# Kernel tuning notes

Hardware: AMD Instinct MI355X
Metric: run time of the kernel (lower is better)

Reference implementation:

```python
import jax, jax.numpy as jnp
import numpy as np

N_NODES = 50000
N_EDGES = 1600000
IN_DIM, HID_DIM, OUT_DIM, HEADS = 128, 128, 64, 8
NEG_SLOPE = 0.2
BN_EPS = 1e-5


def setup_inputs() -> dict:
    key = jax.random.key(0)
    ks = jax.random.split(key, 12)
    hpc = HID_DIM // HEADS  # per-head channels of layer 1
    return {
        "x": jax.random.normal(ks[0], (N_NODES, IN_DIM), jnp.float32),
        "edge_index": jax.random.randint(ks[1], (2, N_EDGES), 0, N_NODES, jnp.int64),
        "W1": jax.random.normal(ks[2], (IN_DIM, HEADS * hpc), jnp.float32) * 0.05,
        "a1_src": jax.random.normal(ks[3], (HEADS, hpc), jnp.float32) * 0.1,
        "a1_dst": jax.random.normal(ks[4], (HEADS, hpc), jnp.float32) * 0.1,
        "b1": jnp.zeros((HEADS * hpc,), jnp.float32),
        "bn_gamma": jnp.ones((HID_DIM,), jnp.float32),
        "bn_beta": jnp.zeros((HID_DIM,), jnp.float32),
        "W2": jax.random.normal(ks[5], (HID_DIM, OUT_DIM), jnp.float32) * 0.05,
        "a2_src": jax.random.normal(ks[6], (1, OUT_DIM), jnp.float32) * 0.1,
        "a2_dst": jax.random.normal(ks[7], (1, OUT_DIM), jnp.float32) * 0.1,
        "b2": jnp.zeros((OUT_DIM,), jnp.float32),
    }


def _gat_conv(x, src, dst, W, a_src, a_dst, bias, heads, n_nodes):
    # x: [N, Fin]; src/dst: [E'] (self-loops already appended)
    hpc = W.shape[1] // heads
    h = (x @ W).reshape(n_nodes, heads, hpc)                 # [N,H,C]
    alpha_s = jnp.einsum("nhc,hc->nh", h, a_src)             # [N,H]
    alpha_d = jnp.einsum("nhc,hc->nh", h, a_dst)
    e = alpha_s[src] + alpha_d[dst]                          # [E',H]
    e = jax.nn.leaky_relu(e, NEG_SLOPE)
    # segment softmax over destination neighborhoods
    m = jax.ops.segment_max(e, dst, num_segments=n_nodes)    # [N,H]
    m = jnp.where(jnp.isfinite(m), m, 0.0)
    ee = jnp.exp(e - m[dst])
    denom = jax.ops.segment_sum(ee, dst, num_segments=n_nodes)
    alpha = ee / (denom[dst] + 1e-16)                        # [E',H]
    msg = h[src] * alpha[:, :, None]                         # [E',H,C]
    out = jax.ops.segment_sum(msg, dst, num_segments=n_nodes)  # [N,H,C]
    return out.reshape(n_nodes, heads * hpc) + bias


def _batch_norm(x, gamma, beta):
    mu = jnp.mean(x, axis=0)
    var = jnp.var(x, axis=0)
    return gamma * (x - mu) * jax.lax.rsqrt(var + BN_EPS) + beta


def reference(x, edge_index, W1, a1_src, a1_dst, b1, bn_gamma, bn_beta, W2, a2_src, a2_dst, b2):
    n = x.shape[0]
    loops = jnp.arange(n, dtype=edge_index.dtype)
    src = jnp.concatenate([edge_index[0], loops])            # PyG add_self_loops
    dst = jnp.concatenate([edge_index[1], loops])
    h = _gat_conv(x, src, dst, W1, a1_src, a1_dst, b1, HEADS, n)
    h = _batch_norm(h, bn_gamma, bn_beta)
    h = jax.nn.elu(h)
    # dropout: identity at inference
    out = _gat_conv(h, src, dst, W2, a2_src, a2_dst, b2, 1, n)
    return out
```

## Files before the change

### kernel.cpp

```cpp
#include <hip/hip_runtime.h>
#include <hip/hip_bf16.h>

#define N_NODES 50000
#define N_EDGES 1600000
#define HEADS 8
#define NBK 196
#define NBLK 196
#define EPB 8192

typedef unsigned short u16;
typedef unsigned char u8;
typedef unsigned int u32;
typedef __attribute__((ext_vector_type(8))) short bf16x8;
typedef __attribute__((ext_vector_type(4))) float f32x4;

__device__ __forceinline__ float bf2f(u16 u) {
  union { u32 i; float f; } v; v.i = ((u32)u) << 16; return v.f;
}
__device__ __forceinline__ float bflo(u32 p) {
  union { u32 i; float f; } v; v.i = p << 16; return v.f;
}
__device__ __forceinline__ float bfhi(u32 p) {
  union { u32 i; float f; } v; v.i = p & 0xffff0000u; return v.f;
}
__device__ __forceinline__ u16 f2bf(float f) {
  union { float f; u32 i; } v; v.f = f;
  u32 r = v.i + 0x7fff + ((v.i >> 16) & 1);
  return (u16)(r >> 16);
}
__device__ __forceinline__ u32 pack2(float a, float b) {
  return (u32)f2bf(a) | ((u32)f2bf(b) << 16);
}
__device__ __forceinline__ int rfl(int x) { return __builtin_amdgcn_readfirstlane(x); }

__global__ void k_detect(const u16* __restrict__ x, const u32* __restrict__ ei,
                         int* __restrict__ flags) {
  __shared__ int cbig, cnz;
  if (threadIdx.x == 0) { cbig = 0; cnz = 0; }
  __syncthreads();
  int lb = 0, ln = 0;
  for (int i = threadIdx.x; i < 4096; i += 256) {
    int ex = (x[i] >> 7) & 0xff;
    lb += (ex >= 140);
    if (i < 2048) ln += (ei[2 * i + 1] != 0);
  }
  atomicAdd(&cbig, lb); atomicAdd(&cnz, ln);
  __syncthreads();
  if (threadIdx.x == 0) {
    flags[0] = (cbig > 16) ? 1 : 0;
    flags[1] = (cnz == 0) ? 1 : 0;
  }
}

__global__ void k_convsmall(const void* a1s, const void* a1d, const void* b1,
                            const void* gam, const void* bet, const void* a2s,
                            const void* a2d, const void* b2, const void* W1,
                            const void* W2, float* __restrict__ smallf,
                            u16* __restrict__ w1t, u16* __restrict__ w2t,
                            const int* __restrict__ flags) {
  int i = blockIdx.x * 256 + threadIdx.x;
  if (i >= 25408) return;
  bool f32 = flags[0] != 0;
  auto ld = [&](const void* p, int off) -> float {
    return f32 ? ((const float*)p)[off] : bf2f(((const u16*)p)[off]);
  };
  if (i >= 17216) {
    int j = i - 17216, n = j >> 7, k = j & 127;
    w2t[j] = f2bf(ld(W2, k * 64 + n));
  } else if (i >= 832) {
    int j = i - 832, n = j >> 7, k = j & 127;
    w1t[j] = f2bf(ld(W1, k * 128 + n));
  } else {
    const void* src; int off;
    if (i >= 768)      { src = b2;  off = i - 768; }
    else if (i >= 704) { src = a2d; off = i - 704; }
    else if (i >= 640) { src = a2s; off = i - 640; }
    else if (i >= 512) { src = bet; off = i - 512; }
    else if (i >= 384) { src = gam; off = i - 384; }
    else if (i >= 256) { src = b1;  off = i - 256; }
    else if (i >= 128) { src = a1d; off = i - 128; }
    else               { src = a1s; off = i; }
    smallf[i] = ld(src, off);
  }
}

__global__ __launch_bounds__(256) void k_hist(const int* __restrict__ ei,
                                              int* __restrict__ H,
                                              int* __restrict__ totals,
                                              const int* __restrict__ flags) {
  __shared__ int hist[NBK];
  int t = threadIdx.x, blk = blockIdx.x;
  for (int i = t; i < NBK; i += 256) hist[i] = 0;
  __syncthreads();
  bool i64 = flags[1] != 0;
  int base = blk * EPB;
  for (int k = 0; k < 32; k++) {
    int e = base + k * 256 + t;
    if (e < N_EDGES) {
      int d = i64 ? ei[2 * (N_EDGES + e)] : ei[N_EDGES + e];
      atomicAdd(&hist[d >> 8], 1);
    }
  }
  __syncthreads();
  for (int i = t; i < NBK; i += 256) {
    H[i * NBLK + blk] = hist[i];
    atomicAdd(&totals[i], hist[i]);
  }
}

__global__ void k_scan_blk(const int* __restrict__ H, const int* __restrict__ totals,
                           int* __restrict__ P) {
  __shared__ int tb[256], tmp[256];
  int t = threadIdx.x, b = blockIdx.x;
  int v0 = (t < NBK) ? totals[t] : 0;
  tb[t] = v0; __syncthreads();
  for (int o = 1; o < 256; o <<= 1) {
    int x = (t >= o) ? tb[t - o] : 0; __syncthreads();
    tb[t] += x; __syncthreads();
  }
  int base = (b == 0) ? 0 : tb[b - 1];
  int v = (t < NBLK) ? H[b * NBLK + t] : 0;
  tmp[t] = v; __syncthreads();
  for (int o = 1; o < 256; o <<= 1) {
    int x = (t >= o) ? tmp[t - o] : 0; __syncthreads();
    tmp[t] += x; __syncthreads();
  }
  if (t < NBLK) P[b * NBLK + t] = base + tmp[t] - v;
}

__global__ __launch_bounds__(256) void k_bucket(const int* __restrict__ ei,
                                                const int* __restrict__ P,
                                                u32* __restrict__ buf,
                                                const int* __restrict__ flags) {
  __shared__ u32 sv[EPB];
  __shared__ u16 rank[EPB];
  __shared__ u8  sk8[EPB];
  __shared__ int cnt[NBK], scn[NBK], tmp[256];
  int t = threadIdx.x, blk = blockIdx.x;
  int base = blk * EPB;
  int nE = N_EDGES - base; if (nE > EPB) nE = EPB;
  for (int i = t; i < NBK; i += 256) cnt[i] = 0;
  __syncthreads();
  bool i64 = flags[1] != 0;
  for (int k = 0; k < EPB / 256; k++) {
    int li = k * 256 + t, e = base + li;
    if (li < nE) {
      int d = i64 ? ei[2 * (N_EDGES + e)] : ei[N_EDGES + e];
      rank[li] = (u16)atomicAdd(&cnt[d >> 8], 1);
    }
  }
  __syncthreads();
  int v = (t < NBK) ? cnt[t] : 0;
  tmp[t] = v; __syncthreads();
  for (int o = 1; o < 256; o <<= 1) {
    int x = (t >= o) ? tmp[t - o] : 0; __syncthreads();
    tmp[t] += x; __syncthreads();
  }
  if (t < NBK) scn[t] = tmp[t] - v;
  __syncthreads();
  for (int k = 0; k < EPB / 256; k++) {
    int li = k * 256 + t, e = base + li;
    if (li < nE) {
      int s = i64 ? ei[2 * e] : ei[e];
      int d = i64 ? ei[2 * (N_EDGES + e)] : ei[N_EDGES + e];
      int key = d >> 8;
      int pos = scn[key] + rank[li];
      sv[pos] = ((u32)(d & 255) << 16) | (u32)s;
      sk8[pos] = (u8)key;
    }
  }
  __syncthreads();
  for (int i = t; i < nE; i += 256) {
    int b = sk8[i];
    buf[P[b * NBLK + blk] + (i - scn[b])] = sv[i];
  }
}

__global__ __launch_bounds__(256) void k_csr(const u32* __restrict__ buf,
                                             const int* __restrict__ totals,
                                             int* __restrict__ row_start,
                                             int* __restrict__ deg,
                                             int* __restrict__ csr, int N) {
  __shared__ int tb[256], cnt[256], scn[256], cur[256];
  int b = blockIdx.x, t = threadIdx.x;
  int v0 = (t < NBK) ? totals[t] : 0;
  tb[t] = v0; __syncthreads();
  for (int o = 1; o < 256; o <<= 1) {
    int x = (t >= o) ? tb[t - o] : 0; __syncthreads();
    tb[t] += x; __syncthreads();
  }
  int lo = (b == 0) ? 0 : tb[b - 1];
  int hi = tb[b];
  cnt[t] = 0; __syncthreads();
  for (int e = lo + t; e < hi; e += 256) atomicAdd(&cnt[(buf[e] >> 16) & 255], 1);
  __syncthreads();
  int v = cnt[t];
  scn[t] = v; __syncthreads();
  for (int o = 1; o < 256; o <<= 1) {
    int x = (t >= o) ? scn[t - o] : 0; __syncthreads();
    scn[t] += x; __syncthreads();
  }
  int excl = scn[t] - v;
  int node = b * 256 + t;
  if (node < N) { row_start[node] = lo + excl; deg[node] = v; }
  cur[t] = lo + excl;
  __syncthreads();
  for (int e = lo + t; e < hi; e += 256) {
    u32 p = buf[e];
    int pos = atomicAdd(&cur[(p >> 16) & 255], 1);
    csr[pos] = p & 0xffff;
  }
}

template <int NCOLS, bool EPI, bool ALPHA1, bool AFLAG>
__global__ __launch_bounds__(256) void k_gemm_mfma(const void* __restrict__ A,
                                                   const u16* __restrict__ BT,
                                                   const float* __restrict__ bnsum,
                                                   const float* __restrict__ bnsq,
                                                   const float* __restrict__ gamma,
                                                   const float* __restrict__ beta,
                                                   const float* __restrict__ va,
                                                   const float* __restrict__ vb,
                                                   float* __restrict__ as_out,
                                                   float* __restrict__ ad_out,
                                                   u16* __restrict__ C, int M,
                                                   const int* __restrict__ flags) {
  constexpr int KP = 136;
  constexpr int NT = NCOLS / 16;
  __shared__ u16 As[64 * KP];
  __shared__ u16 Bs[NCOLS * KP];
  __shared__ float sSc[128], sSh[128];
  int t = threadIdx.x;
  int row0 = blockIdx.x * 64;
  bool af32 = AFLAG ? (flags[0] != 0) : false;

  if (EPI) {
    if (t < 128) {
      float mu = bnsum[t] * (1.f / (float)N_NODES);
      float var = fmaxf(bnsq[t] * (1.f / (float)N_NODES) - mu * mu, 0.f);
      float sc = gamma[t] * rsqrtf(var + 1e-5f);
      sSc[t] = sc; sSh[t] = beta[t] - mu * sc;
    }
    __syncthreads();
  }

  for (int i = t; i < NCOLS * 16; i += 256) {
    int n = i >> 4, q = i & 15;
    *(uint4*)&Bs[n * KP + q * 8] = ((const uint4*)BT)[n * 16 + q];
  }
  for (int i = t; i < 64 * 32; i += 256) {
    int r = i >> 5, c4 = i & 31;
    int row = row0 + r;
    uint2 pk = make_uint2(0u, 0u);
    if (row < M) {
      if (EPI) {
        uint2 p = ((const uint2*)A)[(size_t)row * 32 + c4];
        int c = c4 * 4;
        float v0 = bflo(p.x), v1 = bfhi(p.x), v2 = bflo(p.y), v3 = bfhi(p.y);
        v0 = fmaf(v0, sSc[c],     sSh[c]);     v0 = v0 > 0.f ? v0 : __expf(v0) - 1.f;
        v1 = fmaf(v1, sSc[c + 1], sSh[c + 1]); v1 = v1 > 0.f ? v1 : __expf(v1) - 1.f;
        v2 = fmaf(v2, sSc[c + 2], sSh[c + 2]); v2 = v2 > 0.f ? v2 : __expf(v2) - 1.f;
        v3 = fmaf(v3, sSc[c + 3], sSh[c + 3]); v3 = v3 > 0.f ? v3 : __expf(v3) - 1.f;
        pk.x = pack2(v0, v1); pk.y = pack2(v2, v3);
      } else if (af32) {
        float4 v = ((const float4*)A)[(size_t)row * 32 + c4];
        pk.x = pack2(v.x, v.y); pk.y = pack2(v.z, v.w);
      } else {
        pk = ((const uint2*)A)[(size_t)row * 32 + c4];
      }
    }
    *(uint2*)&As[r * KP + c4 * 4] = pk;
  }
  __syncthreads();

  int lane = t & 63, w = t >> 6;
  int m = lane & 15, quad = lane >> 4;
  f32x4 acc[NT];
#pragma unroll
  for (int nt = 0; nt < NT; nt++) acc[nt] = (f32x4)(0.f);
  const u16* aBase = &As[(w * 16 + m) * KP + quad * 8];
  const u16* bBase = &Bs[m * KP + quad * 8];
#pragma unroll
  for (int ks = 0; ks < 4; ks++) {
    bf16x8 af = *(const bf16x8*)(aBase + ks * 32);
#pragma unroll
    for (int nt = 0; nt < NT; nt++) {
      bf16x8 bf = *(const bf16x8*)(bBase + nt * 16 * KP + ks * 32);
      acc[nt] = __builtin_amdgcn_mfma_f32_16x16x32_bf16(af, bf, acc[nt], 0, 0, 0);
    }
  }
  int orow0 = row0 + w * 16 + quad * 4;
#pragma unroll
  for (int nt = 0; nt < NT; nt++) {
#pragma unroll
    for (int r = 0; r < 4; r++) {
      int row = orow0 + r;
      if (row < M) C[(size_t)row * NCOLS + nt * 16 + m] = f2bf(acc[nt][r]);
    }
  }
  if (ALPHA1) {
    float pav[NT], pbv[NT];
#pragma unroll
    for (int nt = 0; nt < NT; nt++) { pav[nt] = va[nt * 16 + m]; pbv[nt] = vb[nt * 16 + m]; }
#pragma unroll
    for (int r = 0; r < 4; r++) {
      int row = orow0 + r;
#pragma unroll
      for (int nt = 0; nt < NT; nt++) {
        float vs = acc[nt][r] * pav[nt];
        float vd = acc[nt][r] * pbv[nt];
        vs += __shfl_xor(vs, 1); vd += __shfl_xor(vd, 1);
        vs += __shfl_xor(vs, 2); vd += __shfl_xor(vd, 2);
        vs += __shfl_xor(vs, 4); vd += __shfl_xor(vd, 4);
        vs += __shfl_xor(vs, 8); vd += __shfl_xor(vd, 8);
        if (row < M && m == 0) { as_out[row * 8 + nt] = vs; ad_out[row * 8 + nt] = vd; }
      }
    }
  }
  if (EPI) {
    float pav[NT], pbv[NT];
#pragma unroll
    for (int nt = 0; nt < NT; nt++) { pav[nt] = va[nt * 16 + m]; pbv[nt] = vb[nt * 16 + m]; }
#pragma unroll
    for (int r = 0; r < 4; r++) {
      float vs = 0.f, vd = 0.f;
#pragma unroll
      for (int nt = 0; nt < NT; nt++) {
        vs = fmaf(acc[nt][r], pav[nt], vs);
        vd = fmaf(acc[nt][r], pbv[nt], vd);
      }
      vs += __shfl_xor(vs, 1); vd += __shfl_xor(vd, 1);
      vs += __shfl_xor(vs, 2); vd += __shfl_xor(vd, 2);
      vs += __shfl_xor(vs, 4); vd += __shfl_xor(vd, 4);
      vs += __shfl_xor(vs, 8); vd += __shfl_xor(vd, 8);
      int row = orow0 + r;
      if (row < M && m == 0) { as_out[row] = vs; ad_out[row] = vd; }
    }
  }
}

__global__ __launch_bounds__(256) void k_agg1(const u16* __restrict__ h1b,
                                              const float* __restrict__ as_,
                                              const float* __restrict__ ad_,
                                              const int* __restrict__ csr,
                                              const int* __restrict__ row_start,
                                              const int* __restrict__ deg,
                                              const float* __restrict__ b1,
                                              u16* __restrict__ out, int N) {
  int node = blockIdx.x * 4 + (threadIdx.x >> 6);
  if (node >= N) return;
  int l = threadIdx.x & 63;
  int head = l >> 3, sub = l & 7;
  int gbase = l & 56;
  int node_u = rfl(node);
  int st = rfl(row_start[node_u]);
  int cnt = rfl(deg[node_u]);
  const int* cp = csr + st;
  const u32* h32 = (const u32*)h1b;
  float ad = ad_[(node_u << 3) | head];
  float sp = 0.f, a0 = 0.f, a1 = 0.f;
  int j = 0;
  for (; j + 8 <= cnt; j += 8) {
    int ssub = cp[j + sub];
    float e = as_[(ssub << 3) | head] + ad;
    e = fmaxf(e, 0.2f * e);
    float p = __expf(e);
    sp += p;
#pragma unroll
    for (int k = 0; k < 8; k++) {
      int sk = cp[j + k];
      float pk = __shfl(p, gbase | k);
      u32 hv = h32[(sk << 6) | l];
      a0 = fmaf(pk, bflo(hv), a0);
      a1 = fmaf(pk, bfhi(hv), a1);
    }
  }
  for (; j < cnt; j++) {
    int s0 = cp[j];
    float e0 = as_[(s0 << 3) | head] + ad;
    e0 = fmaxf(e0, 0.2f * e0);
    float p0 = __expf(e0);
    if (sub == 0) sp += p0;
    u32 hv = h32[(s0 << 6) | l];
    a0 = fmaf(p0, bflo(hv), a0); a1 = fmaf(p0, bfhi(hv), a1);
  }
  {
    float e0 = as_[(node_u << 3) | head] + ad;
    e0 = fmaxf(e0, 0.2f * e0);
    float p0 = __expf(e0);
    if (sub == 0) sp += p0;
    u32 hv = h32[((size_t)node_u << 6) | l];
    a0 = fmaf(p0, bflo(hv), a0); a1 = fmaf(p0, bfhi(hv), a1);
  }
  sp += __shfl_xor(sp, 1);
  sp += __shfl_xor(sp, 2);
  sp += __shfl_xor(sp, 4);
  float inv = 1.f / (sp + 1e-16f);
  int c0 = l * 2;
  ((u32*)out)[((size_t)node_u << 6) + l] =
      pack2(fmaf(a0, inv, b1[c0]), fmaf(a1, inv, b1[c0 + 1]));
}

__global__ void k_bnstat(const u16* __restrict__ h, float* __restrict__ gsum,
                         float* __restrict__ gsq, int N) {
  __shared__ float ts[256], tq[256];
  int t = threadIdx.x, col = t & 127, rr = t >> 7;
  int row0 = blockIdx.x * 128;
  float s = 0.f, q = 0.f;
  for (int r = rr; r < 128; r += 2) {
    int row = row0 + r;
    if (row < N) {
      float v = bf2f(h[((size_t)row << 7) + col]);
      s += v; q = fmaf(v, v, q);
    }
  }
  ts[t] = s; tq[t] = q; __syncthreads();
  if (t < 128) {
    atomicAdd(&gsum[t], ts[t] + ts[t + 128]);
    atomicAdd(&gsq[t], tq[t] + tq[t + 128]);
  }
}

__global__ __launch_bounds__(256) void k_agg2(const u16* __restrict__ h2b,
                                              const float* __restrict__ as_,
                                              const float* __restrict__ ad_,
                                              const int* __restrict__ csr,
                                              const int* __restrict__ row_start,
                                              const int* __restrict__ deg,
                                              const float* __restrict__ b2,
                                              void* __restrict__ out,
                                              const int* __restrict__ flags, int N) {
  int node = blockIdx.x * 4 + (threadIdx.x >> 6);
  if (node >= N) return;
  int l = threadIdx.x & 63;
  int sub = l & 7, gbase = l & 56;
  int node_u = rfl(node);
  int st = rfl(row_start[node_u]);
  int cnt = rfl(deg[node_u]);
  const int* cp = csr + st;
  float ad = ad_[node_u];
  float sp = 0.f, a = 0.f;
  int j = 0;
  for (; j + 8 <= cnt; j += 8) {
    int ssub = cp[j + sub];
    float e = as_[ssub] + ad;
    e = fmaxf(e, 0.2f * e);
    float p = __expf(e);
    sp += p;
#pragma unroll
    for (int k = 0; k < 8; k++) {
      int sk = cp[j + k];
      float pk = __shfl(p, gbase | k);
      a = fmaf(pk, bf2f((h2b + (sk << 6))[l]), a);
    }
  }
  for (; j < cnt; j++) {
    int s0 = cp[j];
    float e0 = as_[s0] + ad;
    e0 = fmaxf(e0, 0.2f * e0);
    float p0 = __expf(e0);
    if (sub == 0) sp += p0;
    a = fmaf(p0, bf2f((h2b + (s0 << 6))[l]), a);
  }
  {
    float e0 = as_[node_u] + ad;
    e0 = fmaxf(e0, 0.2f * e0);
    float p0 = __expf(e0);
    if (sub == 0) sp += p0;
    a = fmaf(p0, bf2f((h2b + (node_u << 6))[l]), a);
  }
  sp += __shfl_xor(sp, 1);
  sp += __shfl_xor(sp, 2);
  sp += __shfl_xor(sp, 4);
  float r = a / (sp + 1e-16f) + b2[l];
  size_t idx = ((size_t)node_u << 6) + l;
  if (flags[0]) ((float*)out)[idx] = r;
  else          ((u16*)out)[idx] = f2bf(r);
}

extern "C" void kernel_launch(void* const* d_in, const int* in_sizes, int n_in,
                              void* d_out, int out_size, void* d_ws, size_t ws_size,
                              hipStream_t stream) {
  const void* x   = d_in[0];
  const int*  ei  = (const int*)d_in[1];
  const void* W1  = d_in[2];
  const void* a1s = d_in[3];
  const void* a1d = d_in[4];
  const void* b1  = d_in[5];
  const void* gam = d_in[6];
  const void* bet = d_in[7];
  const void* W2  = d_in[8];
  const void* a2s = d_in[9];
  const void* a2d = d_in[10];
  const void* b2  = d_in[11];

  char* ws = (char*)d_ws;
  size_t off = 0;
  auto alloc = [&](size_t bytes) -> void* {
    void* p = ws + off;
    off += (bytes + 255) & ~(size_t)255;
    return p;
  };
  int* flags = (int*)alloc(256);
  char* zreg = (char*)alloc(2048);
  int* totals = (int*)zreg;
  float* gsum = (float*)(zreg + 1024);
  float* gsq  = gsum + 128;
  int* H  = (int*)alloc((size_t)NBK * NBLK * 4);
  int* P  = (int*)alloc((size_t)NBK * NBLK * 4);
  u32* ebuf = (u32*)alloc((size_t)N_EDGES * 4);
  int* csr = (int*)alloc((size_t)N_EDGES * 4);
  int* row_start = (int*)alloc((size_t)N_NODES * 4);
  int* deg = (int*)alloc((size_t)N_NODES * 4);
  float* smallf = (float*)alloc(832 * 4);
  float* a1sf = smallf;        float* a1df = smallf + 128;
  float* b1f  = smallf + 256;  float* gamf = smallf + 384;
  float* betf = smallf + 512;  float* a2sf = smallf + 640;
  float* a2df = smallf + 704;  float* b2f  = smallf + 768;
  u16* w1t = (u16*)alloc(16384 * 2);
  u16* w2t = (u16*)alloc(8192 * 2);
  u16* h1b  = (u16*)alloc((size_t)N_NODES * 128 * 2);
  u16* h1ob = (u16*)alloc((size_t)N_NODES * 128 * 2);
  u16* h2b  = (u16*)alloc((size_t)N_NODES * 64 * 2);
  float* al1s = (float*)alloc((size_t)N_NODES * 8 * 4);
  float* al1d = (float*)alloc((size_t)N_NODES * 8 * 4);
  float* al2s = (float*)alloc((size_t)N_NODES * 4);
  float* al2d = (float*)alloc((size_t)N_NODES * 4);
  if (off > ws_size) return;

  hipMemsetAsync(zreg, 0, 2048, stream);
  k_detect<<<1, 256, 0, stream>>>((const u16*)x, (const u32*)ei, flags);
  k_convsmall<<<100, 256, 0, stream>>>(a1s, a1d, b1, gam, bet, a2s, a2d, b2, W1, W2,
                                       smallf, w1t, w2t, flags);

  k_hist<<<NBLK, 256, 0, stream>>>(ei, H, totals, flags);
  k_scan_blk<<<NBK, 256, 0, stream>>>(H, totals, P);
  k_bucket<<<NBLK, 256, 0, stream>>>(ei, P, ebuf, flags);
  k_csr<<<NBK, 256, 0, stream>>>(ebuf, totals, row_start, deg, csr, N_NODES);

  k_gemm_mfma<128, false, true, true><<<(N_NODES + 63) / 64, 256, 0, stream>>>(
      x, w1t, nullptr, nullptr, nullptr, nullptr, a1sf, a1df, al1s, al1d,
      h1b, N_NODES, flags);
  k_agg1<<<(N_NODES + 3) / 4, 256, 0, stream>>>(h1b, al1s, al1d, csr, row_start, deg,
                                                b1f, h1ob, N_NODES);
  k_bnstat<<<(N_NODES + 127) / 128, 256, 0, stream>>>(h1ob, gsum, gsq, N_NODES);

  k_gemm_mfma<64, true, false, false><<<(N_NODES + 63) / 64, 256, 0, stream>>>(
      h1ob, w2t, gsum, gsq, gamf, betf, a2sf, a2df, al2s, al2d,
      h2b, N_NODES, flags);
  k_agg2<<<(N_NODES + 3) / 4, 256, 0, stream>>>(h2b, al2s, al2d, csr, row_start, deg,
                                                b2f, d_out, flags, N_NODES);
}
```

Before: 334.2 us.

## Reuse histogram ranks in bucketing and fuse BN statistics into layer-1 aggregation

The histogram kernel now stores each edge's in-block rank to a global u16 array, and the bucketing kernel reads those ranks and the per-block histogram instead of re-reading destination indices and redoing shared-memory atomics. The separate batch-norm statistics kernel is removed. Its per-column sum and sum of squares are now accumulated inside k_agg1 through shared-memory atomics followed by global atomics. Aggregation is launched as two halves with a node offset. The change saves a pass over edge destinations and a pass over h1ob, but adds a 3.2 MB rank write and read and many shared-memory float atomics in the aggregation kernel.

```diff
diff --git a/kernel.cpp b/kernel.cpp
--- a/kernel.cpp
+++ b/kernel.cpp
@@ -87,6 +87,7 @@
 __global__ __launch_bounds__(256) void k_hist(const int* __restrict__ ei,
                                               int* __restrict__ H,
                                               int* __restrict__ totals,
+                                              u16* __restrict__ rank16,
                                               const int* __restrict__ flags) {
   __shared__ int hist[NBK];
   int t = threadIdx.x, blk = blockIdx.x;
@@ -98,7 +99,7 @@
     int e = base + k * 256 + t;
     if (e < N_EDGES) {
       int d = i64 ? ei[2 * (N_EDGES + e)] : ei[N_EDGES + e];
-      atomicAdd(&hist[d >> 8], 1);
+      rank16[e] = (u16)atomicAdd(&hist[d >> 8], 1);
     }
   }
   __syncthreads();
@@ -129,28 +130,19 @@
 }
 
 __global__ __launch_bounds__(256) void k_bucket(const int* __restrict__ ei,
+                                                const int* __restrict__ H,
                                                 const int* __restrict__ P,
+                                                const u16* __restrict__ rank16,
                                                 u32* __restrict__ buf,
                                                 const int* __restrict__ flags) {
   __shared__ u32 sv[EPB];
-  __shared__ u16 rank[EPB];
   __shared__ u8  sk8[EPB];
-  __shared__ int cnt[NBK], scn[NBK], tmp[256];
+  __shared__ int scn[NBK], Pl[NBK], tmp[256];
   int t = threadIdx.x, blk = blockIdx.x;
   int base = blk * EPB;
   int nE = N_EDGES - base; if (nE > EPB) nE = EPB;
-  for (int i = t; i < NBK; i += 256) cnt[i] = 0;
-  __syncthreads();
-  bool i64 = flags[1] != 0;
-  for (int k = 0; k < EPB / 256; k++) {
-    int li = k * 256 + t, e = base + li;
-    if (li < nE) {
-      int d = i64 ? ei[2 * (N_EDGES + e)] : ei[N_EDGES + e];
-      rank[li] = (u16)atomicAdd(&cnt[d >> 8], 1);
-    }
-  }
-  __syncthreads();
-  int v = (t < NBK) ? cnt[t] : 0;
+  int v = (t < NBK) ? H[t * NBLK + blk] : 0;
+  if (t < NBK) Pl[t] = P[t * NBLK + blk];
   tmp[t] = v; __syncthreads();
   for (int o = 1; o < 256; o <<= 1) {
     int x = (t >= o) ? tmp[t - o] : 0; __syncthreads();
@@ -158,13 +150,14 @@
   }
   if (t < NBK) scn[t] = tmp[t] - v;
   __syncthreads();
+  bool i64 = flags[1] != 0;
   for (int k = 0; k < EPB / 256; k++) {
     int li = k * 256 + t, e = base + li;
     if (li < nE) {
       int s = i64 ? ei[2 * e] : ei[e];
       int d = i64 ? ei[2 * (N_EDGES + e)] : ei[N_EDGES + e];
       int key = d >> 8;
-      int pos = scn[key] + rank[li];
+      int pos = scn[key] + (int)rank16[e];
       sv[pos] = ((u32)(d & 255) << 16) | (u32)s;
       sk8[pos] = (u8)key;
     }
@@ -172,7 +165,7 @@
   __syncthreads();
   for (int i = t; i < nE; i += 256) {
     int b = sk8[i];
-    buf[P[b * NBLK + blk] + (i - scn[b])] = sv[i];
+    buf[Pl[b] + (i - scn[b])] = sv[i];
   }
 }
 
@@ -346,78 +339,74 @@
                                               const int* __restrict__ row_start,
                                               const int* __restrict__ deg,
                                               const float* __restrict__ b1,
-                                              u16* __restrict__ out, int N) {
-  int node = blockIdx.x * 4 + (threadIdx.x >> 6);
-  if (node >= N) return;
-  int l = threadIdx.x & 63;
-  int head = l >> 3, sub = l & 7;
-  int gbase = l & 56;
-  int node_u = rfl(node);
-  int st = rfl(row_start[node_u]);
-  int cnt = rfl(deg[node_u]);
-  const int* cp = csr + st;
-  const u32* h32 = (const u32*)h1b;
-  float ad = ad_[(node_u << 3) | head];
-  float sp = 0.f, a0 = 0.f, a1 = 0.f;
-  int j = 0;
-  for (; j + 8 <= cnt; j += 8) {
-    int ssub = cp[j + sub];
-    float e = as_[(ssub << 3) | head] + ad;
-    e = fmaxf(e, 0.2f * e);
-    float p = __expf(e);
-    sp += p;
-#pragma unroll
-    for (int k = 0; k < 8; k++) {
-      int sk = cp[j + k];
-      float pk = __shfl(p, gbase | k);
-      u32 hv = h32[(sk << 6) | l];
-      a0 = fmaf(pk, bflo(hv), a0);
-      a1 = fmaf(pk, bfhi(hv), a1);
-    }
-  }
-  for (; j < cnt; j++) {
-    int s0 = cp[j];
-    float e0 = as_[(s0 << 3) | head] + ad;
-    e0 = fmaxf(e0, 0.2f * e0);
-    float p0 = __expf(e0);
-    if (sub == 0) sp += p0;
-    u32 hv = h32[(s0 << 6) | l];
-    a0 = fmaf(p0, bflo(hv), a0); a1 = fmaf(p0, bfhi(hv), a1);
-  }
-  {
-    float e0 = as_[(node_u << 3) | head] + ad;
-    e0 = fmaxf(e0, 0.2f * e0);
-    float p0 = __expf(e0);
-    if (sub == 0) sp += p0;
-    u32 hv = h32[((size_t)node_u << 6) | l];
-    a0 = fmaf(p0, bflo(hv), a0); a1 = fmaf(p0, bfhi(hv), a1);
-  }
-  sp += __shfl_xor(sp, 1);
-  sp += __shfl_xor(sp, 2);
-  sp += __shfl_xor(sp, 4);
-  float inv = 1.f / (sp + 1e-16f);
-  int c0 = l * 2;
-  ((u32*)out)[((size_t)node_u << 6) + l] =
-      pack2(fmaf(a0, inv, b1[c0]), fmaf(a1, inv, b1[c0 + 1]));
-}
-
-__global__ void k_bnstat(const u16* __restrict__ h, float* __restrict__ gsum,
-                         float* __restrict__ gsq, int N) {
-  __shared__ float ts[256], tq[256];
-  int t = threadIdx.x, col = t & 127, rr = t >> 7;
-  int row0 = blockIdx.x * 128;
-  float s = 0.f, q = 0.f;
-  for (int r = rr; r < 128; r += 2) {
-    int row = row0 + r;
-    if (row < N) {
-      float v = bf2f(h[((size_t)row << 7) + col]);
-      s += v; q = fmaf(v, v, q);
-    }
-  }
-  ts[t] = s; tq[t] = q; __syncthreads();
+                                              u16* __restrict__ out,
+                                              float* __restrict__ gsum,
+                                              float* __restrict__ gsq,
+                                              int nodeBase, int N) {
+  __shared__ float lsum[128], lsq[128];
+  int t = threadIdx.x;
+  if (t < 128) { lsum[t] = 0.f; lsq[t] = 0.f; }
+  __syncthreads();
+  int node = nodeBase + blockIdx.x * 4 + (t >> 6);
+  int l = t & 63;
+  if (node < N) {
+    int head = l >> 3, sub = l & 7;
+    int gbase = l & 56;
+    int node_u = rfl(node);
+    int st = rfl(row_start[node_u]);
+    int cnt = rfl(deg[node_u]);
+    const int* cp = csr + st;
+    const u32* h32 = (const u32*)h1b;
+    float ad = ad_[(node_u << 3) | head];
+    float sp = 0.f, a0 = 0.f, a1 = 0.f;
+    int j = 0;
+    for (; j + 8 <= cnt; j += 8) {
+      int ssub = cp[j + sub];
+      float e = as_[(ssub << 3) | head] + ad;
+      e = fmaxf(e, 0.2f * e);
+      float p = __expf(e);
+      sp += p;
+#pragma unroll
+      for (int k = 0; k < 8; k++) {
+        int sk = cp[j + k];
+        float pk = __shfl(p, gbase | k);
+        u32 hv = h32[(sk << 6) | l];
+        a0 = fmaf(pk, bflo(hv), a0);
+        a1 = fmaf(pk, bfhi(hv), a1);
+      }
+    }
+    for (; j < cnt; j++) {
+      int s0 = cp[j];
+      float e0 = as_[(s0 << 3) | head] + ad;
+      e0 = fmaxf(e0, 0.2f * e0);
+      float p0 = __expf(e0);
+      if (sub == 0) sp += p0;
+      u32 hv = h32[(s0 << 6) | l];
+      a0 = fmaf(p0, bflo(hv), a0); a1 = fmaf(p0, bfhi(hv), a1);
+    }
+    {
+      float e0 = as_[(node_u << 3) | head] + ad;
+      e0 = fmaxf(e0, 0.2f * e0);
+      float p0 = __expf(e0);
+      if (sub == 0) sp += p0;
+      u32 hv = h32[((size_t)node_u << 6) | l];
+      a0 = fmaf(p0, bflo(hv), a0); a1 = fmaf(p0, bfhi(hv), a1);
+    }
+    sp += __shfl_xor(sp, 1);
+    sp += __shfl_xor(sp, 2);
+    sp += __shfl_xor(sp, 4);
+    float inv = 1.f / (sp + 1e-16f);
+    int c0 = l * 2;
+    float r0 = fmaf(a0, inv, b1[c0]);
+    float r1 = fmaf(a1, inv, b1[c0 + 1]);
+    ((u32*)out)[((size_t)node_u << 6) + l] = pack2(r0, r1);
+    atomicAdd(&lsum[c0], r0);     atomicAdd(&lsq[c0], r0 * r0);
+    atomicAdd(&lsum[c0 + 1], r1); atomicAdd(&lsq[c0 + 1], r1 * r1);
+  }
+  __syncthreads();
   if (t < 128) {
-    atomicAdd(&gsum[t], ts[t] + ts[t + 128]);
-    atomicAdd(&gsq[t], tq[t] + tq[t + 128]);
+    atomicAdd(&gsum[t], lsum[t]);
+    atomicAdd(&gsq[t], lsq[t]);
   }
 }
 
@@ -508,6 +497,7 @@
   float* gsq  = gsum + 128;
   int* H  = (int*)alloc((size_t)NBK * NBLK * 4);
   int* P  = (int*)alloc((size_t)NBK * NBLK * 4);
+  u16* rank16 = (u16*)alloc((size_t)N_EDGES * 2);
   u32* ebuf = (u32*)alloc((size_t)N_EDGES * 4);
   int* csr = (int*)alloc((size_t)N_EDGES * 4);
   int* row_start = (int*)alloc((size_t)N_NODES * 4);
@@ -533,17 +523,18 @@
   k_convsmall<<<100, 256, 0, stream>>>(a1s, a1d, b1, gam, bet, a2s, a2d, b2, W1, W2,
                                        smallf, w1t, w2t, flags);
 
-  k_hist<<<NBLK, 256, 0, stream>>>(ei, H, totals, flags);
+  k_hist<<<NBLK, 256, 0, stream>>>(ei, H, totals, rank16, flags);
   k_scan_blk<<<NBK, 256, 0, stream>>>(H, totals, P);
-  k_bucket<<<NBLK, 256, 0, stream>>>(ei, P, ebuf, flags);
+  k_bucket<<<NBLK, 256, 0, stream>>>(ei, H, P, rank16, ebuf, flags);
   k_csr<<<NBK, 256, 0, stream>>>(ebuf, totals, row_start, deg, csr, N_NODES);
 
   k_gemm_mfma<128, false, true, true><<<(N_NODES + 63) / 64, 256, 0, stream>>>(
       x, w1t, nullptr, nullptr, nullptr, nullptr, a1sf, a1df, al1s, al1d,
       h1b, N_NODES, flags);
-  k_agg1<<<(N_NODES + 3) / 4, 256, 0, stream>>>(h1b, al1s, al1d, csr, row_start, deg,
-                                                b1f, h1ob, N_NODES);
-  k_bnstat<<<(N_NODES + 127) / 128, 256, 0, stream>>>(h1ob, gsum, gsq, N_NODES);
+  k_agg1<<<6250, 256, 0, stream>>>(h1b, al1s, al1d, csr, row_start, deg,
+                                   b1f, h1ob, gsum, gsq, 0, N_NODES);
+  k_agg1<<<6250, 256, 0, stream>>>(h1b, al1s, al1d, csr, row_start, deg,
+                                   b1f, h1ob, gsum, gsq, 25000, N_NODES);
 
   k_gemm_mfma<64, true, false, false><<<(N_NODES + 63) / 64, 256, 0, stream>>>(
       h1ob, w2t, gsum, gsq, gamf, betf, a2sf, a2df, al2s, al2d,
```

Result: slower. 571.2 us (+70.9%).
